# Optimization experiments

Measured on AMD Instinct MI355X. Metric: run time of the kernel, lower is better.

The kernel has to match this reference:

```python
import jax, jax.numpy as jnp
import numpy as np

EPS = 1e-06

def _feature_map(x):
    # elu(x) + 1, positive feature map
    return jax.nn.elu(x) + 1.0

def setup_inputs() -> dict:
    key = jax.random.key(0)
    k1, k2, k3 = jax.random.split(key, 3)
    B, L, d_k, d_v = 2, 4096, 128, 128
    Q = jax.random.normal(k1, (B, L, d_k), dtype=jnp.float32)
    K = jax.random.normal(k2, (B, L, d_k), dtype=jnp.float32)
    V = jax.random.normal(k3, (B, L, d_v), dtype=jnp.float32)
    return {"Q": Q, "K": K, "V": V}

def reference(Q, K, V):
    # Causal linear attention (ELU feature map).
    # out_l = phi(Q_l) @ sum_{j<=l} phi(K_j)^T V_j
    # Z_l   = phi(Q_l) . sum_{j<=l} phi(K_j)
    phiQ = _feature_map(Q)                       # (B, L, dk)
    phiK = _feature_map(K)                       # (B, L, dk)
    # cumulative KV state: (B, L, dk, dv) -- parallel replacement of the
    # original per-step bmm loop
    KV = jnp.cumsum(phiK[..., :, None] * V[..., None, :], axis=1)
    out = jnp.einsum('blk,blkv->blv', phiQ, KV)  # (B, L, dv)
    Kc = jnp.cumsum(phiK, axis=1)                # (B, L, dk)
    Z = jnp.einsum('blk,blk->bl', phiQ, Kc)[..., None]  # (B, L, 1)
    return out / (Z + EPS)
```

## Files before the change

### kernel.cpp

```cpp
#include <hip/hip_runtime.h>


#define EPS 1e-6f

constexpr int Bc = 2;
constexpr int L  = 4096;
constexpr int D  = 128;
constexpr int C  = 128;
constexpr int NC = L / C;
constexpr int P  = 136;

typedef short sh8 __attribute__((ext_vector_type(8)));
typedef float f4  __attribute__((ext_vector_type(4)));

__device__ __forceinline__ float phi(float x) {
    return x > 0.0f ? x + 1.0f : __expf(x);
}
__device__ __forceinline__ unsigned short f2bf(float f) {
    unsigned u = __float_as_uint(f);
    return (unsigned short)((u + 0x7FFFu + ((u >> 16) & 1u)) >> 16);
}
__device__ __forceinline__ float bf2f(unsigned short h) {
    return __uint_as_float(((unsigned)h) << 16);
}
__device__ __forceinline__ unsigned packbf(float a, float b) {
    return (unsigned)f2bf(a) | ((unsigned)f2bf(b) << 16);
}
__device__ __forceinline__ sh8 splat1() {
    sh8 s;
#pragma unroll
    for (int j = 0; j < 8; ++j) s[j] = (short)0x3F80;
    return s;
}

__global__ __launch_bounds__(512) void k1(
    const float* __restrict__ K, const float* __restrict__ V,
    unsigned short* __restrict__ SB, float* __restrict__ Ksum) {
    const int c = blockIdx.x, b = blockIdx.y, vs = blockIdx.z;
    const int tid = threadIdx.x;
    __shared__ __align__(16) unsigned short sVT[64 * P];
    __shared__ __align__(16) unsigned short sKT[128 * P];
    const size_t base = ((size_t)b * L + (size_t)c * C) * D;

    for (int k = 0; k < 4; ++k) {
        int fi = tid + 512 * k;
        int l = fi >> 4, c4 = fi & 15;
        float4 vd = *(const float4*)(V + base + (size_t)l * D + vs * 64 + c4 * 4);
        int blk = (((l >> 3) + c4) & 15) * 8 + (l & 7);
        sVT[(c4 * 4 + 0) * P + blk] = f2bf(vd.x);
        sVT[(c4 * 4 + 1) * P + blk] = f2bf(vd.y);
        sVT[(c4 * 4 + 2) * P + blk] = f2bf(vd.z);
        sVT[(c4 * 4 + 3) * P + blk] = f2bf(vd.w);
    }
    for (int k = 0; k < 8; ++k) {
        int fi = tid + 512 * k;
        int l = fi >> 5, i4 = fi & 31;
        float4 kd = *(const float4*)(K + base + (size_t)l * D + i4 * 4);
        int blk = (((l >> 3) + i4) & 15) * 8 + (l & 7);
        sKT[(i4 * 4 + 0) * P + blk] = f2bf(phi(kd.x));
        sKT[(i4 * 4 + 1) * P + blk] = f2bf(phi(kd.y));
        sKT[(i4 * 4 + 2) * P + blk] = f2bf(phi(kd.z));
        sKT[(i4 * 4 + 3) * P + blk] = f2bf(phi(kd.w));
    }
    __syncthreads();

    const int w = tid >> 6, lane = tid & 63;
    const int r = lane & 15, q = lane >> 4;
    const int rbase = (w & 3) * 16;
    const int cbase = (w >> 2) * 64;
    const bool doK = ((w & 3) == 0);
    const sh8 ones = splat1();

    f4 acc[4], kz[4];
#pragma unroll
    for (int f = 0; f < 4; ++f) { acc[f] = {0.f,0.f,0.f,0.f}; kz[f] = {0.f,0.f,0.f,0.f}; }
#pragma unroll
    for (int ks = 0; ks < 4; ++ks) {
        int kq = ks * 4 + q;
        int vr = rbase + r;
        sh8 a = *(const sh8*)(sVT + vr * P + ((kq + (vr >> 2)) & 15) * 8);
#pragma unroll
        for (int f = 0; f < 4; ++f) {
            int ir = cbase + f * 16 + r;
            sh8 bk = *(const sh8*)(sKT + ir * P + ((kq + (ir >> 2)) & 15) * 8);
            acc[f] = __builtin_amdgcn_mfma_f32_16x16x32_bf16(a, bk, acc[f], 0, 0, 0);
            if (doK) kz[f] = __builtin_amdgcn_mfma_f32_16x16x32_bf16(ones, bk, kz[f], 0, 0, 0);
        }
    }
    unsigned short* out = SB + ((size_t)(b * NC + c)) * D * D;
#pragma unroll
    for (int f = 0; f < 4; ++f) {
        int i = cbase + f * 16 + r;
#pragma unroll
        for (int e = 0; e < 4; ++e) {
            int v = vs * 64 + rbase + q * 4 + e;
            out[(size_t)v * D + i] = f2bf(acc[f][e]);
        }
    }
    if (doK && q == 0 && vs == 0) {
#pragma unroll
        for (int f = 0; f < 4; ++f)
            Ksum[((size_t)(b * NC + c)) * D + cbase + f * 16 + r] = kz[f][0];
    }
}

__global__ __launch_bounds__(256) void k_scan(unsigned short* __restrict__ SB,
                                              float* __restrict__ Ksum) {
    const int SD = D * D;
    int idx = blockIdx.x * 256 + threadIdx.x;
    if (idx < Bc * SD) {
        int b = idx / SD, e = idx % SD;
        size_t off0 = (size_t)b * NC * SD + e;
        unsigned short vals[NC];
#pragma unroll
        for (int c = 0; c < NC; ++c) vals[c] = SB[off0 + (size_t)c * SD];
        float run = 0.0f;
#pragma unroll
        for (int c = 0; c < NC; ++c) {
            SB[off0 + (size_t)c * SD] = f2bf(run);
            run += bf2f(vals[c]);
        }
    } else if (idx < Bc * SD + Bc * D) {
        int rr = idx - Bc * SD;
        int b = rr >> 7, i = rr & 127;
        size_t off0 = (size_t)b * NC * D + i;
        float vals[NC];
#pragma unroll
        for (int c = 0; c < NC; ++c) vals[c] = Ksum[off0 + (size_t)c * D];
        float run = 0.0f;
#pragma unroll
        for (int c = 0; c < NC; ++c) {
            Ksum[off0 + (size_t)c * D] = run;
            run += vals[c];
        }
    }
}

__global__ __launch_bounds__(512) void k_out(
    const float* __restrict__ Q, const float* __restrict__ K,
    const float* __restrict__ V, const unsigned short* __restrict__ SB,
    const float* __restrict__ Ksum, float* __restrict__ Out) {
    const int c = blockIdx.x, b = blockIdx.y, rs = blockIdx.z;
    const int tid = threadIdx.x;
    __shared__ __align__(16) unsigned short sQ[32 * P];
    __shared__ __align__(16) unsigned short sK[128 * P];
    __shared__ __align__(16) unsigned short sVT[128 * P];
    __shared__ __align__(16) unsigned short sAm[32 * P];
    __shared__ float sZ[32];
    const size_t base  = ((size_t)b * L + (size_t)c * C) * D;
    const size_t tbase = ((size_t)(b * NC + c)) * (size_t)D * D;
    const size_t kb    = ((size_t)(b * NC + c)) * D;

    for (int k = 0; k < 2; ++k) {
        int fi = tid + 512 * k;
        int row = fi >> 5, c4 = fi & 31;
        float4 qd = *(const float4*)(Q + base + (size_t)(rs * 32 + row) * D + c4 * 4);
        uint2 pq; pq.x = packbf(phi(qd.x), phi(qd.y)); pq.y = packbf(phi(qd.z), phi(qd.w));
        *(uint2*)(sQ + row * P + c4 * 4) = pq;
    }
    for (int k = 0; k < 8; ++k) {
        int fi = tid + 512 * k;
        int row = fi >> 5, c4 = fi & 31;
        float4 kd = *(const float4*)(K + base + (size_t)row * D + c4 * 4);
        uint2 pk; pk.x = packbf(phi(kd.x), phi(kd.y)); pk.y = packbf(phi(kd.z), phi(kd.w));
        *(uint2*)(sK + row * P + c4 * 4) = pk;
    }
    for (int k = 0; k < 8; ++k) {
        int fi = tid + 512 * k;
        int l = fi >> 5, i4 = fi & 31;
        float4 vd = *(const float4*)(V + base + (size_t)l * D + i4 * 4);
        int blk = (((l >> 3) + i4) & 15) * 8 + (l & 7);
        sVT[(i4 * 4 + 0) * P + blk] = f2bf(vd.x);
        sVT[(i4 * 4 + 1) * P + blk] = f2bf(vd.y);
        sVT[(i4 * 4 + 2) * P + blk] = f2bf(vd.z);
        sVT[(i4 * 4 + 3) * P + blk] = f2bf(vd.w);
    }
    __syncthreads();

    const int w = tid >> 6, lane = tid & 63;
    const int r = lane & 15, q = lane >> 4;
    const int rbase = (w & 1) * 16;
    const int cq = w >> 1, cbase = cq * 32;
    const bool doZ = (cq == 3);

    sh8 bzk[4];
    if (doZ) {
#pragma unroll
        for (int ks = 0; ks < 4; ++ks) {
            float4 f0 = *(const float4*)(Ksum + kb + ks * 32 + q * 8);
            float4 f1 = *(const float4*)(Ksum + kb + ks * 32 + q * 8 + 4);
            sh8 t;
            t[0] = (short)f2bf(f0.x); t[1] = (short)f2bf(f0.y);
            t[2] = (short)f2bf(f0.z); t[3] = (short)f2bf(f0.w);
            t[4] = (short)f2bf(f1.x); t[5] = (short)f2bf(f1.y);
            t[6] = (short)f2bf(f1.z); t[7] = (short)f2bf(f1.w);
            bzk[ks] = t;
        }
    }

    f4 a2[2];
#pragma unroll
    for (int f = 0; f < 2; ++f) a2[f] = {0.f,0.f,0.f,0.f};
#pragma unroll
    for (int ks = 0; ks < 4; ++ks) {
        sh8 a = *(const sh8*)(sQ + (rbase + r) * P + ks * 32 + q * 8);
#pragma unroll
        for (int f = 0; f < 2; ++f) {
            sh8 bb = *(const sh8*)(sK + (cbase + f * 16 + r) * P + ks * 32 + q * 8);
            a2[f] = __builtin_amdgcn_mfma_f32_16x16x32_bf16(a, bb, a2[f], 0, 0, 0);
        }
    }
#pragma unroll
    for (int f = 0; f < 2; ++f) {
        int j = cbase + f * 16 + r;
#pragma unroll
        for (int e = 0; e < 4; ++e) {
            int lr = rbase + q * 4 + e;
            sAm[lr * P + j] = f2bf((j <= rs * 32 + lr) ? a2[f][e] : 0.f);
        }
    }
    __syncthreads();

    {
        const uint4* sg = (const uint4*)(SB + tbase);
        for (int k = 0; k < 4; ++k) {
            int f2 = tid + 512 * k;
            *(uint4*)(sK + (f2 >> 4) * P + (f2 & 15) * 8) = sg[f2];
        }
    }

    f4 acc[2], zacc = {0.f,0.f,0.f,0.f};
#pragma unroll
    for (int f = 0; f < 2; ++f) acc[f] = {0.f,0.f,0.f,0.f};
    const sh8 ones = splat1();
#pragma unroll
    for (int ks = 0; ks < 4; ++ks) {
        int kq = ks * 4 + q;
        sh8 a = *(const sh8*)(sAm + (rbase + r) * P + ks * 32 + q * 8);
#pragma unroll
        for (int f = 0; f < 2; ++f) {
            int vr = cbase + f * 16 + r;
            sh8 bv = *(const sh8*)(sVT + vr * P + ((kq + (vr >> 2)) & 15) * 8);
            acc[f] = __builtin_amdgcn_mfma_f32_16x16x32_bf16(a, bv, acc[f], 0, 0, 0);
        }
        if (doZ) zacc = __builtin_amdgcn_mfma_f32_16x16x32_bf16(a, ones, zacc, 0, 0, 0);
    }
    __syncthreads();

#pragma unroll
    for (int ks = 0; ks < 4; ++ks) {
        sh8 a = *(const sh8*)(sQ + (rbase + r) * P + ks * 32 + q * 8);
#pragma unroll
        for (int f = 0; f < 2; ++f) {
            sh8 bs = *(const sh8*)(sK + (cbase + f * 16 + r) * P + ks * 32 + q * 8);
            acc[f] = __builtin_amdgcn_mfma_f32_16x16x32_bf16(a, bs, acc[f], 0, 0, 0);
        }
        if (doZ) zacc = __builtin_amdgcn_mfma_f32_16x16x32_bf16(a, bzk[ks], zacc, 0, 0, 0);
    }
    if (doZ && r == 0) {
#pragma unroll
        for (int e = 0; e < 4; ++e) sZ[rbase + q * 4 + e] = zacc[e] + EPS;
    }
    __syncthreads();

#pragma unroll
    for (int f = 0; f < 2; ++f) {
        int v = cbase + f * 16 + r;
#pragma unroll
        for (int e = 0; e < 4; ++e) {
            int lr = rbase + q * 4 + e;
            Out[base + (size_t)(rs * 32 + lr) * D + v] = acc[f][e] / sZ[lr];
        }
    }
}

extern "C" void kernel_launch(void* const* d_in, const int* in_sizes, int n_in,
                              void* d_out, int out_size, void* d_ws, size_t ws_size,
                              hipStream_t stream) {
    const float* Q = (const float*)d_in[0];
    const float* K = (const float*)d_in[1];
    const float* V = (const float*)d_in[2];
    float* Out = (float*)d_out;
    unsigned short* SBw = (unsigned short*)d_ws;
    float* Ksum = (float*)((char*)d_ws + (size_t)Bc * NC * D * D * 2);

    k1<<<dim3(NC, Bc, 2), 512, 0, stream>>>(K, V, SBw, Ksum);
    int total = Bc * D * D + Bc * D;
    k_scan<<<dim3((total + 255) / 256), 256, 0, stream>>>(SBw, Ksum);
    k_out<<<dim3(NC, Bc, 4), 512, 0, stream>>>(Q, K, V, SBw, Ksum, Out);
}
```

Before: 77.74 us.

## Split output kernel into 16-row slices and skip causally masked K/V tiles

The output kernel now uses 256-thread blocks, each handling a 16-row slice of a chunk, and the launch grid grows to 8 slices per chunk. Each block loads and multiplies only the K/V rows up to its causal ceiling, so fully masked tiles are skipped. Every wave computes the normaliser redundantly instead of only one wave, and a reciprocal multiply replaces the shared-memory Z buffer and its barrier. Loading the 128x128 state per block is now repeated across twice as many blocks, which adds global and shared-memory traffic.

```diff
diff --git a/kernel.cpp b/kernel.cpp
--- a/kernel.cpp
+++ b/kernel.cpp
@@ -136,37 +136,36 @@
     }
 }
 
-__global__ __launch_bounds__(512) void k_out(
+__global__ __launch_bounds__(256, 2) void k_out(
     const float* __restrict__ Q, const float* __restrict__ K,
     const float* __restrict__ V, const unsigned short* __restrict__ SB,
     const float* __restrict__ Ksum, float* __restrict__ Out) {
     const int c = blockIdx.x, b = blockIdx.y, rs = blockIdx.z;
     const int tid = threadIdx.x;
-    __shared__ __align__(16) unsigned short sQ[32 * P];
+    __shared__ __align__(16) unsigned short sQ[16 * P];
     __shared__ __align__(16) unsigned short sK[128 * P];
     __shared__ __align__(16) unsigned short sVT[128 * P];
-    __shared__ __align__(16) unsigned short sAm[32 * P];
-    __shared__ float sZ[32];
+    __shared__ __align__(16) unsigned short sAm[16 * P];
     const size_t base  = ((size_t)b * L + (size_t)c * C) * D;
     const size_t tbase = ((size_t)(b * NC + c)) * (size_t)D * D;
     const size_t kb    = ((size_t)(b * NC + c)) * D;
+    const int nrow  = (rs + 1) * 16;
+    const int kceil = min(128, (nrow + 31) & ~31);
 
     for (int k = 0; k < 2; ++k) {
-        int fi = tid + 512 * k;
+        int fi = tid + 256 * k;
         int row = fi >> 5, c4 = fi & 31;
-        float4 qd = *(const float4*)(Q + base + (size_t)(rs * 32 + row) * D + c4 * 4);
+        float4 qd = *(const float4*)(Q + base + (size_t)(rs * 16 + row) * D + c4 * 4);
         uint2 pq; pq.x = packbf(phi(qd.x), phi(qd.y)); pq.y = packbf(phi(qd.z), phi(qd.w));
         *(uint2*)(sQ + row * P + c4 * 4) = pq;
     }
-    for (int k = 0; k < 8; ++k) {
-        int fi = tid + 512 * k;
+    for (int fi = tid; fi < kceil * 32; fi += 256) {
         int row = fi >> 5, c4 = fi & 31;
         float4 kd = *(const float4*)(K + base + (size_t)row * D + c4 * 4);
         uint2 pk; pk.x = packbf(phi(kd.x), phi(kd.y)); pk.y = packbf(phi(kd.z), phi(kd.w));
         *(uint2*)(sK + row * P + c4 * 4) = pk;
     }
-    for (int k = 0; k < 8; ++k) {
-        int fi = tid + 512 * k;
+    for (int fi = tid; fi < kceil * 32; fi += 256) {
         int l = fi >> 5, i4 = fi & 31;
         float4 vd = *(const float4*)(V + base + (size_t)l * D + i4 * 4);
         int blk = (((l >> 3) + i4) & 15) * 8 + (l & 7);
@@ -179,97 +178,87 @@
 
     const int w = tid >> 6, lane = tid & 63;
     const int r = lane & 15, q = lane >> 4;
-    const int rbase = (w & 1) * 16;
-    const int cq = w >> 1, cbase = cq * 32;
-    const bool doZ = (cq == 3);
+    const int cbase = w * 32;
+    int flim = (kceil - cbase + 15) >> 4;
+    flim = flim < 0 ? 0 : (flim > 2 ? 2 : flim);
 
     sh8 bzk[4];
-    if (doZ) {
-#pragma unroll
-        for (int ks = 0; ks < 4; ++ks) {
-            float4 f0 = *(const float4*)(Ksum + kb + ks * 32 + q * 8);
-            float4 f1 = *(const float4*)(Ksum + kb + ks * 32 + q * 8 + 4);
-            sh8 t;
-            t[0] = (short)f2bf(f0.x); t[1] = (short)f2bf(f0.y);
-            t[2] = (short)f2bf(f0.z); t[3] = (short)f2bf(f0.w);
-            t[4] = (short)f2bf(f1.x); t[5] = (short)f2bf(f1.y);
-            t[6] = (short)f2bf(f1.z); t[7] = (short)f2bf(f1.w);
-            bzk[ks] = t;
-        }
+#pragma unroll
+    for (int ks = 0; ks < 4; ++ks) {
+        float4 f0 = *(const float4*)(Ksum + kb + ks * 32 + q * 8);
+        float4 f1 = *(const float4*)(Ksum + kb + ks * 32 + q * 8 + 4);
+        sh8 t;
+        t[0] = (short)f2bf(f0.x); t[1] = (short)f2bf(f0.y);
+        t[2] = (short)f2bf(f0.z); t[3] = (short)f2bf(f0.w);
+        t[4] = (short)f2bf(f1.x); t[5] = (short)f2bf(f1.y);
+        t[6] = (short)f2bf(f1.z); t[7] = (short)f2bf(f1.w);
+        bzk[ks] = t;
     }
 
     f4 a2[2];
-#pragma unroll
-    for (int f = 0; f < 2; ++f) a2[f] = {0.f,0.f,0.f,0.f};
-#pragma unroll
-    for (int ks = 0; ks < 4; ++ks) {
-        sh8 a = *(const sh8*)(sQ + (rbase + r) * P + ks * 32 + q * 8);
-#pragma unroll
-        for (int f = 0; f < 2; ++f) {
+    a2[0] = {0.f,0.f,0.f,0.f}; a2[1] = {0.f,0.f,0.f,0.f};
+#pragma unroll
+    for (int ks = 0; ks < 4; ++ks) {
+        sh8 a = *(const sh8*)(sQ + r * P + ks * 32 + q * 8);
+        for (int f = 0; f < flim; ++f) {
             sh8 bb = *(const sh8*)(sK + (cbase + f * 16 + r) * P + ks * 32 + q * 8);
             a2[f] = __builtin_amdgcn_mfma_f32_16x16x32_bf16(a, bb, a2[f], 0, 0, 0);
         }
     }
-#pragma unroll
-    for (int f = 0; f < 2; ++f) {
+    for (int f = 0; f < flim; ++f) {
         int j = cbase + f * 16 + r;
 #pragma unroll
         for (int e = 0; e < 4; ++e) {
-            int lr = rbase + q * 4 + e;
-            sAm[lr * P + j] = f2bf((j <= rs * 32 + lr) ? a2[f][e] : 0.f);
+            int lr = q * 4 + e;
+            sAm[lr * P + j] = f2bf((j <= rs * 16 + lr) ? a2[f][e] : 0.f);
         }
     }
     __syncthreads();
 
     {
         const uint4* sg = (const uint4*)(SB + tbase);
-        for (int k = 0; k < 4; ++k) {
-            int f2 = tid + 512 * k;
+        for (int k = 0; k < 8; ++k) {
+            int f2 = tid + 256 * k;
             *(uint4*)(sK + (f2 >> 4) * P + (f2 & 15) * 8) = sg[f2];
         }
     }
 
     f4 acc[2], zacc = {0.f,0.f,0.f,0.f};
-#pragma unroll
-    for (int f = 0; f < 2; ++f) acc[f] = {0.f,0.f,0.f,0.f};
+    acc[0] = {0.f,0.f,0.f,0.f}; acc[1] = {0.f,0.f,0.f,0.f};
     const sh8 ones = splat1();
-#pragma unroll
-    for (int ks = 0; ks < 4; ++ks) {
+    const int ks3 = kceil >> 5;
+    for (int ks = 0; ks < ks3; ++ks) {
         int kq = ks * 4 + q;
-        sh8 a = *(const sh8*)(sAm + (rbase + r) * P + ks * 32 + q * 8);
+        sh8 am = *(const sh8*)(sAm + r * P + ks * 32 + q * 8);
 #pragma unroll
         for (int f = 0; f < 2; ++f) {
             int vr = cbase + f * 16 + r;
             sh8 bv = *(const sh8*)(sVT + vr * P + ((kq + (vr >> 2)) & 15) * 8);
-            acc[f] = __builtin_amdgcn_mfma_f32_16x16x32_bf16(a, bv, acc[f], 0, 0, 0);
-        }
-        if (doZ) zacc = __builtin_amdgcn_mfma_f32_16x16x32_bf16(a, ones, zacc, 0, 0, 0);
-    }
-    __syncthreads();
-
-#pragma unroll
-    for (int ks = 0; ks < 4; ++ks) {
-        sh8 a = *(const sh8*)(sQ + (rbase + r) * P + ks * 32 + q * 8);
+            acc[f] = __builtin_amdgcn_mfma_f32_16x16x32_bf16(am, bv, acc[f], 0, 0, 0);
+        }
+        zacc = __builtin_amdgcn_mfma_f32_16x16x32_bf16(am, ones, zacc, 0, 0, 0);
+    }
+    __syncthreads();
+
+#pragma unroll
+    for (int ks = 0; ks < 4; ++ks) {
+        sh8 a = *(const sh8*)(sQ + r * P + ks * 32 + q * 8);
 #pragma unroll
         for (int f = 0; f < 2; ++f) {
             sh8 bs = *(const sh8*)(sK + (cbase + f * 16 + r) * P + ks * 32 + q * 8);
             acc[f] = __builtin_amdgcn_mfma_f32_16x16x32_bf16(a, bs, acc[f], 0, 0, 0);
         }
-        if (doZ) zacc = __builtin_amdgcn_mfma_f32_16x16x32_bf16(a, bzk[ks], zacc, 0, 0, 0);
-    }
-    if (doZ && r == 0) {
-#pragma unroll
-        for (int e = 0; e < 4; ++e) sZ[rbase + q * 4 + e] = zacc[e] + EPS;
-    }
-    __syncthreads();
-
-#pragma unroll
-    for (int f = 0; f < 2; ++f) {
-        int v = cbase + f * 16 + r;
-#pragma unroll
-        for (int e = 0; e < 4; ++e) {
-            int lr = rbase + q * 4 + e;
-            Out[base + (size_t)(rs * 32 + lr) * D + v] = acc[f][e] / sZ[lr];
+        zacc = __builtin_amdgcn_mfma_f32_16x16x32_bf16(a, bzk[ks], zacc, 0, 0, 0);
+    }
+
+#pragma unroll
+    for (int e = 0; e < 4; ++e) {
+        int lr = q * 4 + e;
+        float rz = 1.0f / (zacc[e] + EPS);
+#pragma unroll
+        for (int f = 0; f < 2; ++f) {
+            int v = cbase + f * 16 + r;
+            Out[base + (size_t)(rs * 16 + lr) * D + v] = acc[f][e] * rz;
         }
     }
 }
@@ -287,5 +276,5 @@
     k1<<<dim3(NC, Bc, 2), 512, 0, stream>>>(K, V, SBw, Ksum);
     int total = Bc * D * D + Bc * D;
     k_scan<<<dim3((total + 255) / 256), 256, 0, stream>>>(SBw, Ksum);
-    k_out<<<dim3(NC, Bc, 4), 512, 0, stream>>>(Q, K, V, SBw, Ksum, Out);
-}
+    k_out<<<dim3(NC, Bc, 8), 256, 0, stream>>>(Q, K, V, SBw, Ksum, Out);
+}
```

Measured after the change: 85.75 us. +10.3%, slower.

## Skip causally masked K/V tiles and compute normalizer per wave in k_out

Applied to the files above, without the earlier changes.

In the output kernel, each row-slab block now loads and converts only the K and V rows up to its causal ceiling, and skips the intra-chunk QK^T and AV MFMAs for column tiles that lie entirely above the diagonal. Every wave now computes the Z normalizer itself, which removes the shared sZ buffer and one barrier and replaces the division with a multiply by a reciprocal. The prefix state tile is prefetched into registers at kernel start so its global load overlaps the other loads. Loop trip counts now vary per block, which costs some unrolling, and the redundant Z MFMAs add work to every wave.

```diff
diff --git a/kernel.cpp b/kernel.cpp
--- a/kernel.cpp
+++ b/kernel.cpp
@@ -146,10 +146,17 @@
     __shared__ __align__(16) unsigned short sK[128 * P];
     __shared__ __align__(16) unsigned short sVT[128 * P];
     __shared__ __align__(16) unsigned short sAm[32 * P];
-    __shared__ float sZ[32];
     const size_t base  = ((size_t)b * L + (size_t)c * C) * D;
     const size_t tbase = ((size_t)(b * NC + c)) * (size_t)D * D;
     const size_t kb    = ((size_t)(b * NC + c)) * D;
+    const int kceil = (rs + 1) * 32;
+
+    uint4 sreg[4];
+    {
+        const uint4* sg = (const uint4*)(SB + tbase);
+#pragma unroll
+        for (int k = 0; k < 4; ++k) sreg[k] = sg[tid + 512 * k];
+    }
 
     for (int k = 0; k < 2; ++k) {
         int fi = tid + 512 * k;
@@ -158,15 +165,13 @@
         uint2 pq; pq.x = packbf(phi(qd.x), phi(qd.y)); pq.y = packbf(phi(qd.z), phi(qd.w));
         *(uint2*)(sQ + row * P + c4 * 4) = pq;
     }
-    for (int k = 0; k < 8; ++k) {
-        int fi = tid + 512 * k;
+    for (int fi = tid; fi < kceil * 32; fi += 512) {
         int row = fi >> 5, c4 = fi & 31;
         float4 kd = *(const float4*)(K + base + (size_t)row * D + c4 * 4);
         uint2 pk; pk.x = packbf(phi(kd.x), phi(kd.y)); pk.y = packbf(phi(kd.z), phi(kd.w));
         *(uint2*)(sK + row * P + c4 * 4) = pk;
     }
-    for (int k = 0; k < 8; ++k) {
-        int fi = tid + 512 * k;
+    for (int fi = tid; fi < kceil * 32; fi += 512) {
         int l = fi >> 5, i4 = fi & 31;
         float4 vd = *(const float4*)(V + base + (size_t)l * D + i4 * 4);
         int blk = (((l >> 3) + i4) & 15) * 8 + (l & 7);
@@ -181,37 +186,32 @@
     const int r = lane & 15, q = lane >> 4;
     const int rbase = (w & 1) * 16;
     const int cq = w >> 1, cbase = cq * 32;
-    const bool doZ = (cq == 3);
+    const int flim = (cq <= rs) ? 2 : 0;
 
     sh8 bzk[4];
-    if (doZ) {
-#pragma unroll
-        for (int ks = 0; ks < 4; ++ks) {
-            float4 f0 = *(const float4*)(Ksum + kb + ks * 32 + q * 8);
-            float4 f1 = *(const float4*)(Ksum + kb + ks * 32 + q * 8 + 4);
-            sh8 t;
-            t[0] = (short)f2bf(f0.x); t[1] = (short)f2bf(f0.y);
-            t[2] = (short)f2bf(f0.z); t[3] = (short)f2bf(f0.w);
-            t[4] = (short)f2bf(f1.x); t[5] = (short)f2bf(f1.y);
-            t[6] = (short)f2bf(f1.z); t[7] = (short)f2bf(f1.w);
-            bzk[ks] = t;
-        }
+#pragma unroll
+    for (int ks = 0; ks < 4; ++ks) {
+        float4 f0 = *(const float4*)(Ksum + kb + ks * 32 + q * 8);
+        float4 f1 = *(const float4*)(Ksum + kb + ks * 32 + q * 8 + 4);
+        sh8 t;
+        t[0] = (short)f2bf(f0.x); t[1] = (short)f2bf(f0.y);
+        t[2] = (short)f2bf(f0.z); t[3] = (short)f2bf(f0.w);
+        t[4] = (short)f2bf(f1.x); t[5] = (short)f2bf(f1.y);
+        t[6] = (short)f2bf(f1.z); t[7] = (short)f2bf(f1.w);
+        bzk[ks] = t;
     }
 
     f4 a2[2];
-#pragma unroll
-    for (int f = 0; f < 2; ++f) a2[f] = {0.f,0.f,0.f,0.f};
+    a2[0] = {0.f,0.f,0.f,0.f}; a2[1] = {0.f,0.f,0.f,0.f};
 #pragma unroll
     for (int ks = 0; ks < 4; ++ks) {
         sh8 a = *(const sh8*)(sQ + (rbase + r) * P + ks * 32 + q * 8);
-#pragma unroll
-        for (int f = 0; f < 2; ++f) {
+        for (int f = 0; f < flim; ++f) {
             sh8 bb = *(const sh8*)(sK + (cbase + f * 16 + r) * P + ks * 32 + q * 8);
             a2[f] = __builtin_amdgcn_mfma_f32_16x16x32_bf16(a, bb, a2[f], 0, 0, 0);
         }
     }
-#pragma unroll
-    for (int f = 0; f < 2; ++f) {
+    for (int f = 0; f < flim; ++f) {
         int j = cbase + f * 16 + r;
 #pragma unroll
         for (int e = 0; e < 4; ++e) {
@@ -221,29 +221,25 @@
     }
     __syncthreads();
 
-    {
-        const uint4* sg = (const uint4*)(SB + tbase);
-        for (int k = 0; k < 4; ++k) {
-            int f2 = tid + 512 * k;
-            *(uint4*)(sK + (f2 >> 4) * P + (f2 & 15) * 8) = sg[f2];
-        }
+#pragma unroll
+    for (int k = 0; k < 4; ++k) {
+        int f2 = tid + 512 * k;
+        *(uint4*)(sK + (f2 >> 4) * P + (f2 & 15) * 8) = sreg[k];
     }
 
     f4 acc[2], zacc = {0.f,0.f,0.f,0.f};
-#pragma unroll
-    for (int f = 0; f < 2; ++f) acc[f] = {0.f,0.f,0.f,0.f};
+    acc[0] = {0.f,0.f,0.f,0.f}; acc[1] = {0.f,0.f,0.f,0.f};
     const sh8 ones = splat1();
-#pragma unroll
-    for (int ks = 0; ks < 4; ++ks) {
+    for (int ks = 0; ks <= rs; ++ks) {
         int kq = ks * 4 + q;
-        sh8 a = *(const sh8*)(sAm + (rbase + r) * P + ks * 32 + q * 8);
+        sh8 am = *(const sh8*)(sAm + (rbase + r) * P + ks * 32 + q * 8);
 #pragma unroll
         for (int f = 0; f < 2; ++f) {
             int vr = cbase + f * 16 + r;
             sh8 bv = *(const sh8*)(sVT + vr * P + ((kq + (vr >> 2)) & 15) * 8);
-            acc[f] = __builtin_amdgcn_mfma_f32_16x16x32_bf16(a, bv, acc[f], 0, 0, 0);
-        }
-        if (doZ) zacc = __builtin_amdgcn_mfma_f32_16x16x32_bf16(a, ones, zacc, 0, 0, 0);
+            acc[f] = __builtin_amdgcn_mfma_f32_16x16x32_bf16(am, bv, acc[f], 0, 0, 0);
+        }
+        zacc = __builtin_amdgcn_mfma_f32_16x16x32_bf16(am, ones, zacc, 0, 0, 0);
     }
     __syncthreads();
 
@@ -255,21 +251,17 @@
             sh8 bs = *(const sh8*)(sK + (cbase + f * 16 + r) * P + ks * 32 + q * 8);
             acc[f] = __builtin_amdgcn_mfma_f32_16x16x32_bf16(a, bs, acc[f], 0, 0, 0);
         }
-        if (doZ) zacc = __builtin_amdgcn_mfma_f32_16x16x32_bf16(a, bzk[ks], zacc, 0, 0, 0);
-    }
-    if (doZ && r == 0) {
-#pragma unroll
-        for (int e = 0; e < 4; ++e) sZ[rbase + q * 4 + e] = zacc[e] + EPS;
-    }
-    __syncthreads();
-
-#pragma unroll
-    for (int f = 0; f < 2; ++f) {
-        int v = cbase + f * 16 + r;
-#pragma unroll
-        for (int e = 0; e < 4; ++e) {
-            int lr = rbase + q * 4 + e;
-            Out[base + (size_t)(rs * 32 + lr) * D + v] = acc[f][e] / sZ[lr];
+        zacc = __builtin_amdgcn_mfma_f32_16x16x32_bf16(a, bzk[ks], zacc, 0, 0, 0);
+    }
+
+#pragma unroll
+    for (int e = 0; e < 4; ++e) {
+        int lr = rbase + q * 4 + e;
+        float rz = 1.0f / (zacc[e] + EPS);
+#pragma unroll
+        for (int f = 0; f < 2; ++f) {
+            int v = cbase + f * 16 + r;
+            Out[base + (size_t)(rs * 32 + lr) * D + v] = acc[f][e] * rz;
         }
     }
 }
```

Result: slower. 92.11 us (+18.5%).
